# Kernel tuning notes

Hardware: AMD Instinct MI355X
Metric: run time of the kernel (lower is better)

## Reference

```python
import jax, jax.numpy as jnp
import numpy as np

IN_F = (16, 16, 16)
OUT_F = (16, 16, 16)
RANKS = (8, 8, 8, 8, 8, 8)


def setup_inputs() -> dict:
    key = jax.random.key(0)
    ks = jax.random.split(key, 9)
    x = jax.random.normal(ks[0], (4096, int(np.prod(IN_F))), dtype=jnp.float32)
    # core ~ U[0,1)*0.1 as in torch.rand(ranks)*0.1
    core = jax.random.uniform(ks[1], RANKS, dtype=jnp.float32) * 0.1
    # factor matrices: 3 out-side (out_f[i], r[i]) then 3 in-side (in_f[i], r[i+3])
    shapes = [(OUT_F[i], RANKS[i]) for i in range(3)] + [(IN_F[i], RANKS[i + 3]) for i in range(3)]
    f0, f1, f2, f3, f4, f5 = [
        jax.random.normal(ks[2 + i], shapes[i], dtype=jnp.float32) * 0.1 for i in range(6)
    ]
    bias = jnp.zeros((int(np.prod(OUT_F)),), dtype=jnp.float32)
    return {"x": x, "core": core, "f0": f0, "f1": f1, "f2": f2,
            "f3": f3, "f4": f4, "f5": f5, "bias": bias}


def reference(x, core, f0, f1, f2, f3, f4, f5, bias):
    # x: [N, prod(IN_F)] -> [N, i1, i2, i3]
    xr = x.reshape(-1, *IN_F)
    # Reconstruct full dense weight from Tucker factors (faithful to original)
    # core: [r0..r5]; f0..f2 out-side (out_dim, r); f3..f5 in-side (in_dim, r)
    W = jnp.einsum('ijklmn,ai,bj,ck,dl,em,fn->abcdef', core, f0, f1, f2, f3, f4, f5)
    # Contract input with in-side modes: [N, o1, o2, o3]
    res = jnp.einsum('abcdef,ndef->nabc', W, xr)
    y = res.reshape(-1, int(np.prod(OUT_F)))
    return y + bias
```

## Files before the change

kernel.cpp:

```cpp
#include <hip/hip_runtime.h>

#define THREADS 256

typedef __attribute__((ext_vector_type(8))) short bf16x8;
typedef __attribute__((ext_vector_type(4))) float f32x4;

__device__ inline unsigned short f2bf(float f) {
    union { float f; unsigned int u; } v; v.f = f;
    unsigned int r = v.u + 0x7fffu + ((v.u >> 16) & 1u);
    return (unsigned short)(r >> 16);
}

__global__ __launch_bounds__(THREADS) void k_in_contract(
    const float* __restrict__ x,
    const float* __restrict__ f3, const float* __restrict__ f4,
    const float* __restrict__ f5,
    unsigned short* __restrict__ u3b, int N)
{
    const int n = blockIdx.x;
    const int t = threadIdx.x;

    __shared__ float fs[256];
    __shared__ float u1s[256 * 9];
    __shared__ float u2s[128 * 9];

    if (t < 128) { fs[t] = f3[t]; fs[128 + t] = f4[t]; }

    float xv[16];
    {
        const float4* xr = (const float4*)(x + (size_t)n * 4096 + t * 16);
        float4 a0 = xr[0], a1 = xr[1], a2 = xr[2], a3 = xr[3];
        xv[0]=a0.x; xv[1]=a0.y; xv[2]=a0.z; xv[3]=a0.w;
        xv[4]=a1.x; xv[5]=a1.y; xv[6]=a1.z; xv[7]=a1.w;
        xv[8]=a2.x; xv[9]=a2.y; xv[10]=a2.z; xv[11]=a2.w;
        xv[12]=a3.x; xv[13]=a3.y; xv[14]=a3.z; xv[15]=a3.w;
    }

    float acc8[8];
    #pragma unroll
    for (int q = 0; q < 8; ++q) acc8[q] = 0.f;
    #pragma unroll
    for (int f = 0; f < 16; ++f) {
        const float xf = xv[f];
        #pragma unroll
        for (int n6 = 0; n6 < 8; ++n6)
            acc8[n6] = fmaf(xf, f5[f*8 + n6], acc8[n6]);
    }
    __syncthreads();
    #pragma unroll
    for (int n6 = 0; n6 < 8; ++n6) u1s[t*9 + n6] = acc8[n6];
    __syncthreads();

    {
        const int d = t >> 4, m = (t >> 1) & 7, h = t & 1;
        float fr[16];
        #pragma unroll
        for (int e = 0; e < 16; ++e) fr[e] = fs[128 + e*8 + m];
        float a4[4] = {0.f, 0.f, 0.f, 0.f};
        #pragma unroll
        for (int e = 0; e < 16; ++e) {
            const int base = (d*16 + e)*9 + h*4;
            #pragma unroll
            for (int q = 0; q < 4; ++q)
                a4[q] = fmaf(u1s[base + q], fr[e], a4[q]);
        }
        #pragma unroll
        for (int q = 0; q < 4; ++q) u2s[(d*8 + m)*9 + h*4 + q] = a4[q];
    }
    __syncthreads();

    {
        const int l = t >> 5, m = (t >> 2) & 7, h = t & 3;
        float fr[16];
        #pragma unroll
        for (int d = 0; d < 16; ++d) fr[d] = fs[d*8 + l];
        float a2[2] = {0.f, 0.f};
        #pragma unroll
        for (int d = 0; d < 16; ++d) {
            const int base = (d*8 + m)*9 + h*2;
            a2[0] = fmaf(u2s[base],     fr[d], a2[0]);
            a2[1] = fmaf(u2s[base + 1], fr[d], a2[1]);
        }
        unsigned int pk = (unsigned int)f2bf(a2[0]) |
                          ((unsigned int)f2bf(a2[1]) << 16);
        ((unsigned int*)u3b)[(size_t)n * 256 + t] = pk;
    }
}

__global__ __launch_bounds__(THREADS) void k_convert_core(
    const float* __restrict__ core, unsigned short* __restrict__ coreb)
{
    const int i = blockIdx.x * THREADS + threadIdx.x;
    float4 c = ((const float4*)core)[i];
    ushort4 o;
    o.x = f2bf(c.x); o.y = f2bf(c.y); o.z = f2bf(c.z); o.w = f2bf(c.w);
    ((ushort4*)coreb)[i] = o;
}

__global__ __launch_bounds__(THREADS) void k_core_gemm_mfma(
    const unsigned short* __restrict__ u3b,
    const unsigned short* __restrict__ coreb,
    float* __restrict__ v, int N)
{
    const int t    = threadIdx.x;
    const int lane = t & 63;
    const int wave = t >> 6;
    const int m0 = blockIdx.x * 128 + wave * 32;
    const int p0 = blockIdx.y * 32;
    const int lr = lane & 15;
    const int lq = lane >> 4;

    const unsigned short* aptr0 = u3b   + (size_t)(m0 + lr) * 512 + lq * 8;
    const unsigned short* aptr1 = aptr0 + 16 * 512;
    const unsigned short* bptr0 = coreb + (size_t)(p0 + lr) * 512 + lq * 8;
    const unsigned short* bptr1 = bptr0 + 16 * 512;

    f32x4 acc00 = {0.f,0.f,0.f,0.f}, acc01 = {0.f,0.f,0.f,0.f};
    f32x4 acc10 = {0.f,0.f,0.f,0.f}, acc11 = {0.f,0.f,0.f,0.f};

    #pragma unroll
    for (int k0 = 0; k0 < 512; k0 += 32) {
        bf16x8 a0 = *(const bf16x8*)(aptr0 + k0);
        bf16x8 a1 = *(const bf16x8*)(aptr1 + k0);
        bf16x8 b0 = *(const bf16x8*)(bptr0 + k0);
        bf16x8 b1 = *(const bf16x8*)(bptr1 + k0);
        acc00 = __builtin_amdgcn_mfma_f32_16x16x32_bf16(a0, b0, acc00, 0, 0, 0);
        acc01 = __builtin_amdgcn_mfma_f32_16x16x32_bf16(a0, b1, acc01, 0, 0, 0);
        acc10 = __builtin_amdgcn_mfma_f32_16x16x32_bf16(a1, b0, acc10, 0, 0, 0);
        acc11 = __builtin_amdgcn_mfma_f32_16x16x32_bf16(a1, b1, acc11, 0, 0, 0);
    }

    const int row = m0 + lq * 4;
    const int col = p0 + lr;
    #pragma unroll
    for (int r = 0; r < 4; ++r) {
        v[(size_t)(row + r) * 512 + col]           = acc00[r];
        v[(size_t)(row + r) * 512 + col + 16]      = acc01[r];
        v[(size_t)(row + 16 + r) * 512 + col]      = acc10[r];
        v[(size_t)(row + 16 + r) * 512 + col + 16] = acc11[r];
    }
}

__global__ __launch_bounds__(THREADS) void k_out_expand5(
    const float* __restrict__ v,
    const float* __restrict__ f0, const float* __restrict__ f1,
    const float* __restrict__ f2, const float* __restrict__ bias,
    float* __restrict__ y, int N)
{
    const int n = blockIdx.x;
    const int t = threadIdx.x;

    __shared__ float fs[256];
    __shared__ float vs[512];
    __shared__ float w1s[128 * 9];
    __shared__ float w2s[8 * 257];

    if (t < 128) { fs[t] = f0[t]; fs[128 + t] = f1[t]; }
    if (t < 128) ((float4*)vs)[t] = ((const float4*)(v + (size_t)n*512))[t];

    float f2r[32];
    {
        const float4* fp = (const float4*)(f2 + ((t & 3) * 4) * 8);
        #pragma unroll
        for (int q8 = 0; q8 < 8; ++q8) {
            float4 ff = fp[q8];
            f2r[q8*4+0] = ff.x; f2r[q8*4+1] = ff.y;
            f2r[q8*4+2] = ff.z; f2r[q8*4+3] = ff.w;
        }
    }
    __syncthreads();

    {
        const int a = t >> 4, j = (t >> 1) & 7, h = t & 1;
        float fr[8];
        #pragma unroll
        for (int i = 0; i < 8; ++i) fr[i] = fs[a*8 + i];
        float a4[4] = {0.f, 0.f, 0.f, 0.f};
        #pragma unroll
        for (int i = 0; i < 8; ++i) {
            const int base = i*64 + j*8 + h*4;
            #pragma unroll
            for (int q = 0; q < 4; ++q)
                a4[q] = fmaf(vs[base + q], fr[i], a4[q]);
        }
        #pragma unroll
        for (int q = 0; q < 4; ++q) w1s[(a*8 + j)*9 + h*4 + q] = a4[q];
    }
    __syncthreads();

    {
        const int a = t >> 4, b = t & 15;
        float fr[8];
        #pragma unroll
        for (int j = 0; j < 8; ++j) fr[j] = fs[128 + b*8 + j];
        float w2[8] = {0.f,0.f,0.f,0.f,0.f,0.f,0.f,0.f};
        #pragma unroll
        for (int j = 0; j < 8; ++j) {
            const int base = (a*8 + j)*9;
            const float fj = fr[j];
            #pragma unroll
            for (int k = 0; k < 8; ++k)
                w2[k] = fmaf(w1s[base + k], fj, w2[k]);
        }
        #pragma unroll
        for (int k = 0; k < 8; ++k) w2s[k*257 + t] = w2[k];
    }
    __syncthreads();

    {
        const int w = t >> 6;
        const int B = (t >> 2) & 15;
        const float4* bias4 = (const float4*)bias;
        float4* y4 = (float4*)(y + (size_t)n * 4096);

        #pragma unroll
        for (int s = 0; s < 4; ++s) {
            const int AB = (s*4 + w) * 16 + B;
            float w2v[8];
            #pragma unroll
            for (int k = 0; k < 8; ++k) w2v[k] = w2s[k*257 + AB];

            float4 bb = bias4[s*256 + t];
            float r0 = bb.x, r1 = bb.y, r2 = bb.z, r3 = bb.w;
            #pragma unroll
            for (int k = 0; k < 8; ++k) {
                r0 = fmaf(w2v[k], f2r[0*8 + k], r0);
                r1 = fmaf(w2v[k], f2r[1*8 + k], r1);
                r2 = fmaf(w2v[k], f2r[2*8 + k], r2);
                r3 = fmaf(w2v[k], f2r[3*8 + k], r3);
            }
            y4[s*256 + t] = make_float4(r0, r1, r2, r3);
        }
    }
}

extern "C" void kernel_launch(void* const* d_in, const int* in_sizes, int n_in,
                              void* d_out, int out_size, void* d_ws, size_t ws_size,
                              hipStream_t stream)
{
    const float* x    = (const float*)d_in[0];
    const float* core = (const float*)d_in[1];
    const float* f0   = (const float*)d_in[2];
    const float* f1   = (const float*)d_in[3];
    const float* f2   = (const float*)d_in[4];
    const float* f3   = (const float*)d_in[5];
    const float* f4   = (const float*)d_in[6];
    const float* f5   = (const float*)d_in[7];
    const float* bias = (const float*)d_in[8];
    float* y = (float*)d_out;

    const int N = in_sizes[0] / 4096;

    unsigned short* u3b   = (unsigned short*)d_ws;
    unsigned short* coreb = u3b + (size_t)N * 512;
    float*          v     = (float*)(coreb + 512 * 512);

    k_in_contract<<<N, THREADS, 0, stream>>>(x, f3, f4, f5, u3b, N);
    k_convert_core<<<256, THREADS, 0, stream>>>(core, coreb);
    dim3 gb(N / 128, 512 / 32);
    k_core_gemm_mfma<<<gb, THREADS, 0, stream>>>(u3b, coreb, v, N);
    k_out_expand5<<<N, THREADS, 0, stream>>>(v, f0, f1, f2, bias, y, N);
}
```

Before: 161.5 us.

## Process four rows per block in out-expand kernel with prefetch and lighter barriers

The output-expansion kernel now handles four batch rows per block instead of one. It loads factors and bias once per block and prefetches the next row's v vector into registers during the current row's compute. Plain __syncthreads is replaced by a custom LDS barrier built from a waitcnt, s_barrier and a sched_barrier. This amortizes setup loads and launch overhead and hides global latency, at the cost of fewer blocks (N/4) and more serialized work per block.

```diff
diff --git a/kernel.cpp b/kernel.cpp
--- a/kernel.cpp
+++ b/kernel.cpp
@@ -9,6 +9,12 @@
     union { float f; unsigned int u; } v; v.f = f;
     unsigned int r = v.u + 0x7fffu + ((v.u >> 16) & 1u);
     return (unsigned short)(r >> 16);
+}
+
+__device__ inline void lds_barrier() {
+    asm volatile("s_waitcnt lgkmcnt(0)" ::: "memory");
+    __builtin_amdgcn_s_barrier();
+    __builtin_amdgcn_sched_barrier(0);
 }
 
 __global__ __launch_bounds__(THREADS) void k_in_contract(
@@ -141,14 +147,14 @@
     }
 }
 
-__global__ __launch_bounds__(THREADS) void k_out_expand5(
+__global__ __launch_bounds__(THREADS) void k_out_expand6(
     const float* __restrict__ v,
     const float* __restrict__ f0, const float* __restrict__ f1,
     const float* __restrict__ f2, const float* __restrict__ bias,
     float* __restrict__ y, int N)
 {
-    const int n = blockIdx.x;
-    const int t = threadIdx.x;
+    const int t  = threadIdx.x;
+    const int r0 = blockIdx.x * 4;
 
     __shared__ float fs[256];
     __shared__ float vs[512];
@@ -156,7 +162,7 @@
     __shared__ float w2s[8 * 257];
 
     if (t < 128) { fs[t] = f0[t]; fs[128 + t] = f1[t]; }
-    if (t < 128) ((float4*)vs)[t] = ((const float4*)(v + (size_t)n*512))[t];
+    if (t < 128) ((float4*)vs)[t] = ((const float4*)(v + (size_t)r0 * 512))[t];
 
     float f2r[32];
     {
@@ -168,69 +174,84 @@
             f2r[q8*4+2] = ff.z; f2r[q8*4+3] = ff.w;
         }
     }
-    __syncthreads();
-
-    {
-        const int a = t >> 4, j = (t >> 1) & 7, h = t & 1;
-        float fr[8];
-        #pragma unroll
-        for (int i = 0; i < 8; ++i) fr[i] = fs[a*8 + i];
-        float a4[4] = {0.f, 0.f, 0.f, 0.f};
-        #pragma unroll
-        for (int i = 0; i < 8; ++i) {
-            const int base = i*64 + j*8 + h*4;
-            #pragma unroll
-            for (int q = 0; q < 4; ++q)
-                a4[q] = fmaf(vs[base + q], fr[i], a4[q]);
-        }
-        #pragma unroll
-        for (int q = 0; q < 4; ++q) w1s[(a*8 + j)*9 + h*4 + q] = a4[q];
-    }
-    __syncthreads();
-
-    {
-        const int a = t >> 4, b = t & 15;
-        float fr[8];
-        #pragma unroll
-        for (int j = 0; j < 8; ++j) fr[j] = fs[128 + b*8 + j];
-        float w2[8] = {0.f,0.f,0.f,0.f,0.f,0.f,0.f,0.f};
-        #pragma unroll
-        for (int j = 0; j < 8; ++j) {
-            const int base = (a*8 + j)*9;
-            const float fj = fr[j];
-            #pragma unroll
-            for (int k = 0; k < 8; ++k)
-                w2[k] = fmaf(w1s[base + k], fj, w2[k]);
-        }
-        #pragma unroll
-        for (int k = 0; k < 8; ++k) w2s[k*257 + t] = w2[k];
-    }
-    __syncthreads();
-
-    {
-        const int w = t >> 6;
-        const int B = (t >> 2) & 15;
-        const float4* bias4 = (const float4*)bias;
-        float4* y4 = (float4*)(y + (size_t)n * 4096);
-
-        #pragma unroll
-        for (int s = 0; s < 4; ++s) {
-            const int AB = (s*4 + w) * 16 + B;
-            float w2v[8];
-            #pragma unroll
-            for (int k = 0; k < 8; ++k) w2v[k] = w2s[k*257 + AB];
-
-            float4 bb = bias4[s*256 + t];
-            float r0 = bb.x, r1 = bb.y, r2 = bb.z, r3 = bb.w;
-            #pragma unroll
-            for (int k = 0; k < 8; ++k) {
-                r0 = fmaf(w2v[k], f2r[0*8 + k], r0);
-                r1 = fmaf(w2v[k], f2r[1*8 + k], r1);
-                r2 = fmaf(w2v[k], f2r[2*8 + k], r2);
-                r3 = fmaf(w2v[k], f2r[3*8 + k], r3);
+    const float4* bias4 = (const float4*)bias;
+    float4 bb0 = bias4[0*256 + t], bb1 = bias4[1*256 + t];
+    float4 bb2 = bias4[2*256 + t], bb3 = bias4[3*256 + t];
+
+    lds_barrier();
+
+    const int a_ = t >> 4, j_ = (t >> 1) & 7, h_ = t & 1;
+    const int b_ = t & 15;
+    const int w_ = t >> 6, B_ = (t >> 2) & 15;
+
+    float fr0[8], fr1[8];
+    #pragma unroll
+    for (int i = 0; i < 8; ++i) fr0[i] = fs[a_*8 + i];
+    #pragma unroll
+    for (int j = 0; j < 8; ++j) fr1[j] = fs[128 + b_*8 + j];
+
+    #pragma unroll 1
+    for (int rr = 0; rr < 4; ++rr) {
+        const int n = r0 + rr;
+
+        float4 vpf = make_float4(0.f, 0.f, 0.f, 0.f);
+        if (rr < 3 && t < 128)
+            vpf = ((const float4*)(v + (size_t)(n + 1) * 512))[t];
+
+        {
+            float a4[4] = {0.f, 0.f, 0.f, 0.f};
+            #pragma unroll
+            for (int i = 0; i < 8; ++i) {
+                const int base = i*64 + j_*8 + h_*4;
+                const float fi = fr0[i];
+                #pragma unroll
+                for (int q = 0; q < 4; ++q)
+                    a4[q] = fmaf(vs[base + q], fi, a4[q]);
             }
-            y4[s*256 + t] = make_float4(r0, r1, r2, r3);
-        }
+            #pragma unroll
+            for (int q = 0; q < 4; ++q) w1s[(a_*8 + j_)*9 + h_*4 + q] = a4[q];
+        }
+        lds_barrier();
+
+        {
+            float w2[8] = {0.f,0.f,0.f,0.f,0.f,0.f,0.f,0.f};
+            #pragma unroll
+            for (int j = 0; j < 8; ++j) {
+                const int base = (a_*8 + j)*9;
+                const float fj = fr1[j];
+                #pragma unroll
+                for (int k = 0; k < 8; ++k)
+                    w2[k] = fmaf(w1s[base + k], fj, w2[k]);
+            }
+            #pragma unroll
+            for (int k = 0; k < 8; ++k) w2s[k*257 + t] = w2[k];
+        }
+        if (rr < 3 && t < 128) ((float4*)vs)[t] = vpf;
+        lds_barrier();
+
+        {
+            float4* y4 = (float4*)(y + (size_t)n * 4096);
+            #pragma unroll
+            for (int s = 0; s < 4; ++s) {
+                const int AB = (s*4 + w_) * 16 + B_;
+                float w2v[8];
+                #pragma unroll
+                for (int k = 0; k < 8; ++k) w2v[k] = w2s[k*257 + AB];
+
+                float4 bb = (s == 0) ? bb0 : (s == 1) ? bb1
+                          : (s == 2) ? bb2 : bb3;
+                float rv0 = bb.x, rv1 = bb.y, rv2 = bb.z, rv3 = bb.w;
+                #pragma unroll
+                for (int k = 0; k < 8; ++k) {
+                    rv0 = fmaf(w2v[k], f2r[0*8 + k], rv0);
+                    rv1 = fmaf(w2v[k], f2r[1*8 + k], rv1);
+                    rv2 = fmaf(w2v[k], f2r[2*8 + k], rv2);
+                    rv3 = fmaf(w2v[k], f2r[3*8 + k], rv3);
+                }
+                y4[s*256 + t] = make_float4(rv0, rv1, rv2, rv3);
+            }
+        }
+        lds_barrier();
     }
 }
 
@@ -259,5 +280,5 @@
     k_convert_core<<<256, THREADS, 0, stream>>>(core, coreb);
     dim3 gb(N / 128, 512 / 32);
     k_core_gemm_mfma<<<gb, THREADS, 0, stream>>>(u3b, coreb, v, N);
-    k_out_expand5<<<N, THREADS, 0, stream>>>(v, f0, f1, f2, bias, y, N);
-}
+    k_out_expand6<<<N / 4, THREADS, 0, stream>>>(v, f0, f1, f2, bias, y, N);
+}
```

New measurement: 153.3 us. 1.05x faster.
